# Kernel optimization log

Measured on AMD Instinct MI355X. Metric: run time of the kernel, lower is better.

The kernel has to match this reference:

```python
import jax, jax.numpy as jnp
import numpy as np

GDEP = 2
ALPHA = 0.05

def setup_inputs() -> dict:
    key = jax.random.key(0)
    ks = jax.random.split(key, 6)
    B, C, V, L = 8, 32, 512, 256  # L = c_in * num_patterns
    x = jax.random.normal(ks[0], (B, C, V, L), dtype=jnp.float32)
    adj = jax.random.uniform(ks[1], (B, V, V), dtype=jnp.float32)
    W = jax.random.normal(ks[2], (L, L), dtype=jnp.float32) * (1.0 / np.sqrt(L))
    b = jax.random.normal(ks[3], (L,), dtype=jnp.float32) * (1.0 / np.sqrt(L))
    conv_w = jax.random.normal(ks[4], (C, (GDEP + 1) * C, 1, 1), dtype=jnp.float32) * 0.1
    conv_b = jax.random.normal(ks[5], (C,), dtype=jnp.float32) * 0.1
    return {"x": x, "adj": adj, "W": W, "b": b, "conv_w": conv_w, "conv_b": conv_b}

def reference(x, adj, W, b, conv_w, conv_b):
    B, C, V, L = x.shape
    # adj normalization: add self loops, divide by column-sums (sum over dim 1)
    adj_new = adj + jnp.eye(V, dtype=adj.dtype)[None]          # [B,V,V]
    d = adj_new.sum(axis=1)[:, None, :]                        # [B,1,V]
    a = adj_new / d                                            # [B,V,V]
    h = x
    out = [h]
    for _ in range(GDEP):
        hw = h @ W + b                                         # [B,C,V,L] (matmul on last dim)
        diff = jnp.einsum('ncwl,nvw->ncvl', hw, a)             # hypergraph diffusion over nodes
        h = ALPHA * x + (1.0 - ALPHA) * diff
        out.append(h)
    ho = jnp.concatenate(out, axis=1)                          # [B,(gdep+1)*C,V,L]
    # 1x1 Conv2d == channel-mixing einsum
    w2 = conv_w[:, :, 0, 0]                                    # [C_out, (gdep+1)*C]
    ho = jnp.einsum('bcvl,oc->bovl', ho, w2) + conv_b[None, :, None, None]
    return ho
```

## Files before the change

### kernel.cpp

```cpp
#include <hip/hip_runtime.h>

constexpr int NB = 8;
constexpr int NC = 32;
constexpr int NV = 512;
constexpr int NL = 256;
constexpr float F_ALPHA = 0.05f;
constexpr float F_BETA  = 0.95f;

typedef __bf16 bf16x8 __attribute__((ext_vector_type(8)));
typedef float  f32x4  __attribute__((ext_vector_type(4)));

__device__ __forceinline__ void async_ld16(const void* g, void* l) {
  __builtin_amdgcn_global_load_lds(
      (const __attribute__((address_space(1))) void*)g,
      (__attribute__((address_space(3))) void*)l, 16, 0, 0);
}


__global__ void k_colsum_part(const float* __restrict__ adj, float* __restrict__ partial) {
  int idx = blockIdx.x * 256 + threadIdx.x;
  int w = idx & 511;
  int chunk = (idx >> 9) & 7;
  int n = idx >> 12;
  const float* p = adj + n * (NV * NV) + chunk * 64 * NV + w;
  float s = 0.f;
#pragma unroll
  for (int v = 0; v < 64; ++v) s += p[v * NV];
  partial[idx] = s;
}

__global__ void k_dinv(const float* __restrict__ partial, float* __restrict__ dinv) {
  int idx = blockIdx.x * 256 + threadIdx.x;
  int w = idx & 511;
  int n = idx >> 9;
  float s = 1.f;
#pragma unroll
  for (int j = 0; j < 8; ++j) s += partial[n * 4096 + j * 512 + w];
  dinv[idx] = 1.f / s;
}

__global__ void k_prep_a(const float* __restrict__ adj, const float* __restrict__ dinv,
                         __bf16* __restrict__ a) {
  int idx = blockIdx.x * 256 + threadIdx.x;
  int w = idx & 511;
  int v = (idx >> 9) & 511;
  int n = idx >> 18;
  float val = adj[idx] + (v == w ? 1.0f : 0.0f);
  a[idx] = (__bf16)(val * dinv[(n << 9) | w]);
}

__global__ void k_prep_wt(const float* __restrict__ W, __bf16* __restrict__ Wt) {
  int idx = blockIdx.x * 256 + threadIdx.x;
  int l = idx >> 8, k = idx & 255;
  Wt[idx] = (__bf16)W[(k << 8) | l];
}

template <bool BF32>
__global__ __launch_bounds__(256, 2)
void k_gemm_wt(const __bf16* __restrict__ Wt, const void* __restrict__ Bsrc,
               const float* __restrict__ bias, __bf16* __restrict__ hw) {
  __shared__ __align__(16) char lds[32768];
  char* ldsA = lds;
  char* ldsB = lds + 16384;

  const int tid = threadIdx.x;
  const int bid = blockIdx.x;
  const int p = bid >> 3;
  const int mtile = (bid >> 2) & 1;
  const int ntile = bid & 3;
  const int n = p >> 5, c = p & 31;

  int Bbase, Bstride;
  if (BF32) { Bbase = p * (NV * NL); Bstride = NL; }
  else      { Bbase = n * (NV * NC * NL) + c * NL; Bstride = NC * NL; }

  const int wave = tid >> 6, lane = tid & 63;
  const int quad = lane >> 4, l16 = lane & 15;
  const int wm = wave >> 1, wn = wave & 1;
  const int wbase = (tid & ~63) * 16;

  f32x4 acc[4][4];
#pragma unroll
  for (int i = 0; i < 4; ++i)
#pragma unroll
    for (int j = 0; j < 4; ++j) acc[i][j] = (f32x4){0.f, 0.f, 0.f, 0.f};

  for (int kt = 0; kt < 256 / 64; ++kt) {
    __syncthreads();
#pragma unroll
    for (int j = 0; j < 4; ++j) {
      int pos = j * 4096 + tid * 16;
      int row = pos >> 7;
      int kb = (pos & 127) ^ ((row & 7) * 16);
      const __bf16* g = Wt + (mtile * 128 + row) * 256 + kt * 64 + (kb >> 1);
      async_ld16(g, ldsA + j * 4096 + wbase);
    }
    if (BF32) {
      const float* Bf = (const float*)Bsrc;
#pragma unroll
      for (int j = 0; j < 4; ++j) {
        int pos = j * 4096 + tid * 16;
        int row = pos >> 7;
        int kb = (pos & 127) ^ ((row & 7) * 16);
        const float* g = Bf + Bbase + (ntile * 128 + row) * Bstride + kt * 64 + (kb >> 1);
        float4 f0 = *(const float4*)g;
        float4 f1 = *(const float4*)(g + 4);
        bf16x8 vv;
        vv[0] = (__bf16)f0.x; vv[1] = (__bf16)f0.y; vv[2] = (__bf16)f0.z; vv[3] = (__bf16)f0.w;
        vv[4] = (__bf16)f1.x; vv[5] = (__bf16)f1.y; vv[6] = (__bf16)f1.z; vv[7] = (__bf16)f1.w;
        *(bf16x8*)(ldsB + pos) = vv;
      }
    } else {
      const __bf16* Bf = (const __bf16*)Bsrc;
#pragma unroll
      for (int j = 0; j < 4; ++j) {
        int pos = j * 4096 + tid * 16;
        int row = pos >> 7;
        int kb = (pos & 127) ^ ((row & 7) * 16);
        const __bf16* g = Bf + Bbase + (ntile * 128 + row) * Bstride + kt * 64 + (kb >> 1);
        async_ld16(g, ldsB + j * 4096 + wbase);
      }
    }
    __syncthreads();
#pragma unroll
    for (int ks = 0; ks < 2; ++ks) {
      bf16x8 af[4], bfr[4];
#pragma unroll
      for (int mb = 0; mb < 4; ++mb) {
        int m = wm * 64 + mb * 16 + l16;
        int kb = (ks * 64 + quad * 16) ^ ((m & 7) * 16);
        af[mb] = *(const bf16x8*)(ldsA + m * 128 + kb);
      }
#pragma unroll
      for (int nb = 0; nb < 4; ++nb) {
        int nn = wn * 64 + nb * 16 + l16;
        int kb = (ks * 64 + quad * 16) ^ ((nn & 7) * 16);
        bfr[nb] = *(const bf16x8*)(ldsB + nn * 128 + kb);
      }
#pragma unroll
      for (int mb = 0; mb < 4; ++mb)
#pragma unroll
        for (int nb = 0; nb < 4; ++nb)
          acc[mb][nb] = __builtin_amdgcn_mfma_f32_16x16x32_bf16(af[mb], bfr[nb], acc[mb][nb], 0, 0, 0);
    }
  }
  __bf16* outp = hw + p * (NL * NV) + mtile * 128 * NV + ntile * 128;
#pragma unroll
  for (int mb = 0; mb < 4; ++mb) {
#pragma unroll
    for (int r = 0; r < 4; ++r) {
      int ml = wm * 64 + mb * 16 + quad * 4 + r;
      float bv = bias[mtile * 128 + ml];
#pragma unroll
      for (int nb = 0; nb < 4; ++nb) {
        int nl = wn * 64 + nb * 16 + l16;
        outp[ml * NV + nl] = (__bf16)(acc[mb][nb][r] + bv);
      }
    }
  }
}

__global__ __launch_bounds__(256, 2)
void k_gemm_a(const __bf16* __restrict__ abuf, const __bf16* __restrict__ hw,
              const float* __restrict__ x, __bf16* __restrict__ hout) {
  __shared__ __align__(16) char lds[32768];
  char* ldsA = lds;
  char* ldsB = lds + 16384;

  const int tid = threadIdx.x;
  const int bid = blockIdx.x;
  const int n = bid >> 8;
  const int mtile = (bid >> 6) & 3;
  const int ntile = bid & 63;

  const __bf16* Ab = abuf + n * (NV * NV) + mtile * 128 * NV;
  const __bf16* Bb = hw + n * (NC * NL * NV) + ntile * 128 * NV;

  const int wave = tid >> 6, lane = tid & 63;
  const int quad = lane >> 4, l16 = lane & 15;
  const int wm = wave >> 1, wn = wave & 1;
  const int wbase = (tid & ~63) * 16;

  f32x4 acc[4][4];
#pragma unroll
  for (int i = 0; i < 4; ++i)
#pragma unroll
    for (int j = 0; j < 4; ++j) acc[i][j] = (f32x4){0.f, 0.f, 0.f, 0.f};

  for (int kt = 0; kt < 512 / 64; ++kt) {
    __syncthreads();
#pragma unroll
    for (int j = 0; j < 4; ++j) {
      int pos = j * 4096 + tid * 16;
      int row = pos >> 7;
      int kb = (pos & 127) ^ ((row & 7) * 16);
      async_ld16(Ab + row * NV + kt * 64 + (kb >> 1), ldsA + j * 4096 + wbase);
    }
#pragma unroll
    for (int j = 0; j < 4; ++j) {
      int pos = j * 4096 + tid * 16;
      int row = pos >> 7;
      int kb = (pos & 127) ^ ((row & 7) * 16);
      async_ld16(Bb + row * NV + kt * 64 + (kb >> 1), ldsB + j * 4096 + wbase);
    }
    __syncthreads();
#pragma unroll
    for (int ks = 0; ks < 2; ++ks) {
      bf16x8 af[4], bfr[4];
#pragma unroll
      for (int mb = 0; mb < 4; ++mb) {
        int m = wm * 64 + mb * 16 + l16;
        int kb = (ks * 64 + quad * 16) ^ ((m & 7) * 16);
        af[mb] = *(const bf16x8*)(ldsA + m * 128 + kb);
      }
#pragma unroll
      for (int nb = 0; nb < 4; ++nb) {
        int nn = wn * 64 + nb * 16 + l16;
        int kb = (ks * 64 + quad * 16) ^ ((nn & 7) * 16);
        bfr[nb] = *(const bf16x8*)(ldsB + nn * 128 + kb);
      }
#pragma unroll
      for (int mb = 0; mb < 4; ++mb)
#pragma unroll
        for (int nb = 0; nb < 4; ++nb)
          acc[mb][nb] = __builtin_amdgcn_mfma_f32_16x16x32_bf16(af[mb], bfr[nb], acc[mb][nb], 0, 0, 0);
    }
  }
#pragma unroll
  for (int mb = 0; mb < 4; ++mb) {
#pragma unroll
    for (int r = 0; r < 4; ++r) {
      int v = mtile * 128 + wm * 64 + mb * 16 + quad * 4 + r;
#pragma unroll
      for (int nb = 0; nb < 4; ++nb) {
        int col = ntile * 128 + wn * 64 + nb * 16 + l16;
        int c = col >> 8, l = col & 255;
        float xv = x[((n * NC + c) * NV + v) * NL + l];
        hout[n * (NV * NC * NL) + v * (NC * NL) + col] =
            (__bf16)(F_ALPHA * xv + F_BETA * acc[mb][nb][r]);
      }
    }
  }
}

__global__ __launch_bounds__(256, 2)
void k_conv(const float* __restrict__ x, const __bf16* __restrict__ h1,
            const __bf16* __restrict__ h2, const float* __restrict__ cw,
            const float* __restrict__ cb, float* __restrict__ out) {
  __shared__ __align__(16) char lds[288 * 208];
  char* Bt = lds;
  char* Aw = lds + 256 * 208;

  const int tid = threadIdx.x;
  const int bid = blockIdx.x;
  const int n = bid >> 9, v = bid & 511;

  for (int i = tid; i < 3072; i += 256) {
    int o = i / 96, k = i - o * 96;
    *(__bf16*)(Aw + o * 208 + k * 2) = (__bf16)cw[i];
  }

  {
    const int l = tid;
    bf16x8 pk;
    const float* xp = x + n * (NC * NV * NL) + v * NL + l;
#pragma unroll
    for (int c = 0; c < 32; ++c) {
      pk[c & 7] = (__bf16)xp[c * (NV * NL)];
      if ((c & 7) == 7) *(bf16x8*)(Bt + l * 208 + (c - 7) * 2) = pk;
    }
    const __bf16* hp1 = h1 + (n * NV + v) * (NC * NL) + l;
#pragma unroll
    for (int c = 0; c < 32; ++c) {
      pk[c & 7] = hp1[c * NL];
      if ((c & 7) == 7) *(bf16x8*)(Bt + l * 208 + (32 + c - 7) * 2) = pk;
    }
    const __bf16* hp2 = h2 + (n * NV + v) * (NC * NL) + l;
#pragma unroll
    for (int c = 0; c < 32; ++c) {
      pk[c & 7] = hp2[c * NL];
      if ((c & 7) == 7) *(bf16x8*)(Bt + l * 208 + (64 + c - 7) * 2) = pk;
    }
  }
  __syncthreads();

  const int wave = tid >> 6, lane = tid & 63;
  const int quad = lane >> 4, l16 = lane & 15;

  f32x4 acc[2][4];
#pragma unroll
  for (int i = 0; i < 2; ++i)
#pragma unroll
    for (int j = 0; j < 4; ++j) acc[i][j] = (f32x4){0.f, 0.f, 0.f, 0.f};

#pragma unroll
  for (int ks = 0; ks < 3; ++ks) {
    bf16x8 af[2], bfr[4];
#pragma unroll
    for (int mt = 0; mt < 2; ++mt) {
      int m = mt * 16 + l16;
      af[mt] = *(const bf16x8*)(Aw + m * 208 + ks * 64 + quad * 16);
    }
#pragma unroll
    for (int nb = 0; nb < 4; ++nb) {
      int ll = wave * 64 + nb * 16 + l16;
      bfr[nb] = *(const bf16x8*)(Bt + ll * 208 + ks * 64 + quad * 16);
    }
#pragma unroll
    for (int mt = 0; mt < 2; ++mt)
#pragma unroll
      for (int nb = 0; nb < 4; ++nb)
        acc[mt][nb] = __builtin_amdgcn_mfma_f32_16x16x32_bf16(af[mt], bfr[nb], acc[mt][nb], 0, 0, 0);
  }

#pragma unroll
  for (int mt = 0; mt < 2; ++mt) {
#pragma unroll
    for (int r = 0; r < 4; ++r) {
      int o = mt * 16 + quad * 4 + r;
      float bo = cb[o];
#pragma unroll
      for (int nb = 0; nb < 4; ++nb) {
        int ll = wave * 64 + nb * 16 + l16;
        out[((n * NC + o) * NV + v) * NL + ll] = acc[mt][nb][r] + bo;
      }
    }
  }
}

extern "C" void kernel_launch(void* const* d_in, const int* in_sizes, int n_in,
                              void* d_out, int out_size, void* d_ws, size_t ws_size,
                              hipStream_t stream) {
  const float* x   = (const float*)d_in[0];
  const float* adj = (const float*)d_in[1];
  const float* W   = (const float*)d_in[2];
  const float* b   = (const float*)d_in[3];
  const float* cw  = (const float*)d_in[4];
  const float* cb  = (const float*)d_in[5];
  float* out = (float*)d_out;
  char* ws = (char*)d_ws;

  float*  dinv    = (float*)ws;
  float*  partial = (float*)(ws + 16384);
  __bf16* Wt      = (__bf16*)(ws + 147456);
  __bf16* abuf    = (__bf16*)(ws + 278528);
  __bf16* hwbuf   = (__bf16*)(ws + 4472832);
  __bf16* h1      = (__bf16*)(ws + 4472832 + 67108864);
  __bf16* h2      = (__bf16*)(ws + 4472832 + 2 * 67108864);

  k_colsum_part<<<128, 256, 0, stream>>>(adj, partial);
  k_dinv<<<16, 256, 0, stream>>>(partial, dinv);
  k_prep_a<<<8192, 256, 0, stream>>>(adj, dinv, abuf);
  k_prep_wt<<<256, 256, 0, stream>>>(W, Wt);

  k_gemm_wt<true><<<2048, 256, 0, stream>>>(Wt, (const void*)x, b, hwbuf);
  k_gemm_a<<<2048, 256, 0, stream>>>(abuf, hwbuf, x, h1);
  k_gemm_wt<false><<<2048, 256, 0, stream>>>(Wt, (const void*)h1, b, hwbuf);
  k_gemm_a<<<2048, 256, 0, stream>>>(abuf, hwbuf, x, h2);

  k_conv<<<4096, 256, 0, stream>>>(x, h1, h2, cw, cb, out);
}
```

Baseline: 508.1 us.

## Drop x reads from diffusion epilogue by folding alpha*x into conv weights

The diffusion GEMM no longer reads fp32 x in its epilogue; it stores only the raw diffusion result D. The alpha*x terms are folded algebraically: into the conv weights (precomputed cwF, with the x-channel weights absorbing alpha times the h1/h2 weights), and into the second W-GEMM, whose epilogue blends alpha times the previous hw (which equals x@W+b) with beta times the new product. This removes the scattered fp32 x loads in both diffusion epilogues but adds a bf16 read of hwA in the second W-GEMM epilogue. Buffers are reused across slots, and the rounding order shifts slightly.

```diff
diff --git a/kernel.cpp b/kernel.cpp
--- a/kernel.cpp
+++ b/kernel.cpp
@@ -55,10 +55,22 @@
   Wt[idx] = (__bf16)W[(k << 8) | l];
 }
 
-template <bool BF32>
+__global__ void k_prep_cwf(const float* __restrict__ cw, float* __restrict__ cwF) {
+  int idx = blockIdx.x * 256 + threadIdx.x;
+  if (idx < 3072) {
+    int o = idx / 96, k = idx - o * 96;
+    float v;
+    if (k < 32)      v = cw[o * 96 + k] + F_ALPHA * (cw[o * 96 + 32 + k] + cw[o * 96 + 64 + k]);
+    else             v = F_BETA * cw[o * 96 + k];
+    cwF[idx] = v;
+  }
+}
+
+template <bool BF32, int EPI>
 __global__ __launch_bounds__(256, 2)
 void k_gemm_wt(const __bf16* __restrict__ Wt, const void* __restrict__ Bsrc,
-               const float* __restrict__ bias, __bf16* __restrict__ hw) {
+               const float* __restrict__ bias, __bf16* __restrict__ hw,
+               const __bf16* __restrict__ hwprev) {
   __shared__ __align__(16) char lds[32768];
   char* ldsA = lds;
   char* ldsB = lds + 16384;
@@ -144,7 +156,9 @@
           acc[mb][nb] = __builtin_amdgcn_mfma_f32_16x16x32_bf16(af[mb], bfr[nb], acc[mb][nb], 0, 0, 0);
     }
   }
-  __bf16* outp = hw + p * (NL * NV) + mtile * 128 * NV + ntile * 128;
+  const size_t obase = (size_t)p * (NL * NV) + mtile * 128 * NV + ntile * 128;
+  __bf16* outp = hw + obase;
+  const __bf16* prevp = (EPI == 1) ? hwprev + obase : nullptr;
 #pragma unroll
   for (int mb = 0; mb < 4; ++mb) {
 #pragma unroll
@@ -154,7 +168,12 @@
 #pragma unroll
       for (int nb = 0; nb < 4; ++nb) {
         int nl = wn * 64 + nb * 16 + l16;
-        outp[ml * NV + nl] = (__bf16)(acc[mb][nb][r] + bv);
+        if (EPI == 0) {
+          outp[ml * NV + nl] = (__bf16)(acc[mb][nb][r] + bv);
+        } else {
+          float pv = (float)prevp[ml * NV + nl];
+          outp[ml * NV + nl] = (__bf16)(F_ALPHA * pv + F_BETA * (acc[mb][nb][r] + bv));
+        }
       }
     }
   }
@@ -162,7 +181,7 @@
 
 __global__ __launch_bounds__(256, 2)
 void k_gemm_a(const __bf16* __restrict__ abuf, const __bf16* __restrict__ hw,
-              const float* __restrict__ x, __bf16* __restrict__ hout) {
+              __bf16* __restrict__ dout) {
   __shared__ __align__(16) char lds[32768];
   char* ldsA = lds;
   char* ldsB = lds + 16384;
@@ -234,18 +253,15 @@
 #pragma unroll
       for (int nb = 0; nb < 4; ++nb) {
         int col = ntile * 128 + wn * 64 + nb * 16 + l16;
-        int c = col >> 8, l = col & 255;
-        float xv = x[((n * NC + c) * NV + v) * NL + l];
-        hout[n * (NV * NC * NL) + v * (NC * NL) + col] =
-            (__bf16)(F_ALPHA * xv + F_BETA * acc[mb][nb][r]);
+        dout[n * (NV * NC * NL) + v * (NC * NL) + col] = (__bf16)acc[mb][nb][r];
       }
     }
   }
 }
 
 __global__ __launch_bounds__(256, 2)
-void k_conv(const float* __restrict__ x, const __bf16* __restrict__ h1,
-            const __bf16* __restrict__ h2, const float* __restrict__ cw,
+void k_conv(const float* __restrict__ x, const __bf16* __restrict__ d1,
+            const __bf16* __restrict__ d2, const float* __restrict__ cwF,
             const float* __restrict__ cb, float* __restrict__ out) {
   __shared__ __align__(16) char lds[288 * 208];
   char* Bt = lds;
@@ -257,7 +273,7 @@
 
   for (int i = tid; i < 3072; i += 256) {
     int o = i / 96, k = i - o * 96;
-    *(__bf16*)(Aw + o * 208 + k * 2) = (__bf16)cw[i];
+    *(__bf16*)(Aw + o * 208 + k * 2) = (__bf16)cwF[i];
   }
 
   {
@@ -269,13 +285,13 @@
       pk[c & 7] = (__bf16)xp[c * (NV * NL)];
       if ((c & 7) == 7) *(bf16x8*)(Bt + l * 208 + (c - 7) * 2) = pk;
     }
-    const __bf16* hp1 = h1 + (n * NV + v) * (NC * NL) + l;
+    const __bf16* hp1 = d1 + (n * NV + v) * (NC * NL) + l;
 #pragma unroll
     for (int c = 0; c < 32; ++c) {
       pk[c & 7] = hp1[c * NL];
       if ((c & 7) == 7) *(bf16x8*)(Bt + l * 208 + (32 + c - 7) * 2) = pk;
     }
-    const __bf16* hp2 = h2 + (n * NV + v) * (NC * NL) + l;
+    const __bf16* hp2 = d2 + (n * NV + v) * (NC * NL) + l;
 #pragma unroll
     for (int c = 0; c < 32; ++c) {
       pk[c & 7] = hp2[c * NL];
@@ -344,19 +360,25 @@
   float*  partial = (float*)(ws + 16384);
   __bf16* Wt      = (__bf16*)(ws + 147456);
   __bf16* abuf    = (__bf16*)(ws + 278528);
-  __bf16* hwbuf   = (__bf16*)(ws + 4472832);
-  __bf16* h1      = (__bf16*)(ws + 4472832 + 67108864);
-  __bf16* h2      = (__bf16*)(ws + 4472832 + 2 * 67108864);
+  __bf16* slot1   = (__bf16*)(ws + 4472832);
+  __bf16* slot2   = (__bf16*)(ws + 4472832 + 67108864);
+  __bf16* slot3   = (__bf16*)(ws + 4472832 + 2 * 67108864);
+  float*  cwF     = partial;
+
+  __bf16* hwA = slot1;
+  __bf16* D1  = slot2;
+  __bf16* hwB = slot3;
+  __bf16* D2  = slot1;
 
   k_colsum_part<<<128, 256, 0, stream>>>(adj, partial);
   k_dinv<<<16, 256, 0, stream>>>(partial, dinv);
+  k_prep_cwf<<<12, 256, 0, stream>>>(cw, cwF);
   k_prep_a<<<8192, 256, 0, stream>>>(adj, dinv, abuf);
   k_prep_wt<<<256, 256, 0, stream>>>(W, Wt);
 
-  k_gemm_wt<true><<<2048, 256, 0, stream>>>(Wt, (const void*)x, b, hwbuf);
-  k_gemm_a<<<2048, 256, 0, stream>>>(abuf, hwbuf, x, h1);
-  k_gemm_wt<false><<<2048, 256, 0, stream>>>(Wt, (const void*)h1, b, hwbuf);
-  k_gemm_a<<<2048, 256, 0, stream>>>(abuf, hwbuf, x, h2);
-
-  k_conv<<<4096, 256, 0, stream>>>(x, h1, h2, cw, cb, out);
-}
+  k_gemm_wt<true, 0><<<2048, 256, 0, stream>>>(Wt, (const void*)x, b, hwA, nullptr);
+  k_gemm_a<<<2048, 256, 0, stream>>>(abuf, hwA, D1);
+  k_gemm_wt<false, 1><<<2048, 256, 0, stream>>>(Wt, (const void*)D1, b, hwB, hwA);
+  k_gemm_a<<<2048, 256, 0, stream>>>(abuf, hwB, D2);
+  k_conv<<<4096, 256, 0, stream>>>(x, D1, D2, cwF, cb, out);
+}
```

New measurement: 457.1 us. 10.0% less time.
